# Kernel optimization log

Measured on AMD Instinct MI355X. Metric: run time of the kernel, lower is better.

The kernel has to match this reference:

```python
import jax, jax.numpy as jnp
import numpy as np

VOCAB = 2048
HID = 1024
BATCH = 64
STEPS = 512


def setup_inputs() -> dict:
    key = jax.random.key(0)
    ks = jax.random.split(key, 4)
    return {
        "X": jax.random.randint(ks[0], (BATCH, STEPS), 0, VOCAB, dtype=jnp.int64 if jax.config.read('jax_enable_x64') else jnp.int32),
        "state_h": jnp.zeros((BATCH, HID), dtype=jnp.float32),
        "W_xh": jax.random.normal(ks[1], (VOCAB, HID), dtype=jnp.float32) * 0.01,
        "W_hh": jax.random.normal(ks[2], (HID, HID), dtype=jnp.float32) * 0.01,
        "b_h": jnp.zeros((HID,), dtype=jnp.float32),
        "W_hq": jax.random.normal(ks[3], (HID, VOCAB), dtype=jnp.float32) * 0.01,
        "b_q": jnp.zeros((VOCAB,), dtype=jnp.float32),
    }


def reference(X, state_h, W_xh, W_hh, b_h, W_hq, b_q):
    # X: [B, T] int; one-hot of X.T -> [T, B, V] float32 (as in F.one_hot(X.T, V))
    Xoh = jax.nn.one_hot(X.T, VOCAB, dtype=jnp.float32)

    def step(H, x_t):
        # x_t: [B, V]; H: [B, H]
        H_new = jnp.tanh(x_t @ W_xh + H @ W_hh + b_h)
        Y_t = H_new @ W_hq + b_q  # [B, V]
        return H_new, Y_t

    H_final, Ys = jax.lax.scan(step, state_h, Xoh)  # Ys: [T, B, V]
    # torch.cat(outputs, dim=0) -> [T*B, V]
    Y = Ys.reshape(STEPS * BATCH, VOCAB)
    return Y, H_final
```

## Files before the change

kernel.cpp:

```cpp
#include <hip/hip_runtime.h>
#include <hip/hip_bf16.h>


#define BSZ  64
#define TSTEPS 512
#define HID  1024
#define VOC  2048

typedef __attribute__((ext_vector_type(8))) __bf16 bf16x8;
typedef __attribute__((ext_vector_type(4))) float  f32x4;

#define HALL_BYTES  67239936ull
#define WT_BYTES     4194304ull
#define FLAGS_BYTES   131328ull

__device__ inline void async_load16(const void* g, void* l) {
    __builtin_amdgcn_global_load_lds(
        (const __attribute__((address_space(1))) void*)g,
        (__attribute__((address_space(3))) void*)l, 16, 0, 0);
}

__device__ inline void load8_l2(const __hip_bfloat16* base, bf16x8* a) {
    asm volatile(
        "global_load_dwordx4 %0, %8, off sc0\n\t"
        "global_load_dwordx4 %1, %8, off offset:64 sc0\n\t"
        "global_load_dwordx4 %2, %8, off offset:128 sc0\n\t"
        "global_load_dwordx4 %3, %8, off offset:192 sc0\n\t"
        "global_load_dwordx4 %4, %8, off offset:256 sc0\n\t"
        "global_load_dwordx4 %5, %8, off offset:320 sc0\n\t"
        "global_load_dwordx4 %6, %8, off offset:384 sc0\n\t"
        "global_load_dwordx4 %7, %8, off offset:448 sc0"
        : "=&v"(a[0]), "=&v"(a[1]), "=&v"(a[2]), "=&v"(a[3]),
          "=&v"(a[4]), "=&v"(a[5]), "=&v"(a[6]), "=&v"(a[7])
        : "v"(base)
        : "memory");
}

__device__ inline void store_bf16_wt(__hip_bfloat16* p, float v) {
    const __hip_bfloat16 hv = __float2bfloat16(v);
    __hip_atomic_store((unsigned short*)p, __builtin_bit_cast(unsigned short, hv),
                       __ATOMIC_RELAXED, __HIP_MEMORY_SCOPE_SYSTEM);
}

__global__ __launch_bounds__(256, 1) void rnn_phase1(
    const int* __restrict__ X, const float* __restrict__ h0,
    const float* __restrict__ W_xh, const float* __restrict__ W_hh,
    const float* __restrict__ b_h,
    __hip_bfloat16* __restrict__ Hall, float* __restrict__ Hfin,
    unsigned int* __restrict__ flags)
{
    __builtin_amdgcn_fence(__ATOMIC_ACQUIRE, "agent");

    const int wg   = blockIdx.x;
    const int j0   = wg * 16;
    const int tid  = threadIdx.x;
    const int wave = tid >> 6;
    const int lane = tid & 63;
    const int lrow = lane & 15;
    const int lq   = lane >> 4;
    const int row0 = wave * 16;

    bf16x8 Bfr[32];
#pragma unroll
    for (int ks = 0; ks < 32; ++ks) {
        const int kb = ks * 32 + lq * 8;
        bf16x8 v;
#pragma unroll
        for (int j = 0; j < 8; ++j)
            v[j] = (__bf16)W_hh[(size_t)(kb + j) * HID + j0 + lrow];
        Bfr[ks] = v;
    }
    const float bh = b_h[j0 + lrow];

    for (int i = tid; i < BSZ * 16; i += 256) {
        const int b = i >> 4, c = i & 15;
        store_bf16_wt(Hall + (size_t)b * HID + j0 + c, h0[(size_t)b * HID + j0 + c]);
    }
    asm volatile("s_waitcnt vmcnt(0)" ::: "memory");
    __syncthreads();
    if (tid == 0)
        __hip_atomic_store(&flags[wg], 1u, __ATOMIC_RELAXED, __HIP_MEMORY_SCOPE_SYSTEM);

    for (int t = 0; t < TSTEPS; ++t) {
        float g[4];
#pragma unroll
        for (int r = 0; r < 4; ++r) {
            const int b = row0 + lq * 4 + r;
            const int x = X[b * TSTEPS + t];
            g[r] = W_xh[(size_t)x * HID + j0 + lrow];
        }
        {
            unsigned int* fl = flags + (size_t)t * 64;
            int guard = 0;
            while (__hip_atomic_load(&fl[lane], __ATOMIC_RELAXED, __HIP_MEMORY_SCOPE_SYSTEM) == 0u) {
                __builtin_amdgcn_s_sleep(1);
                if (++guard > (1 << 13)) break;
            }
        }

        const __hip_bfloat16* Arow =
            Hall + (size_t)t * (BSZ * HID) + (size_t)(row0 + lrow) * HID + lq * 8;
        bf16x8 a[32];
        load8_l2(Arow,       a);
        load8_l2(Arow + 256, a + 8);
        load8_l2(Arow + 512, a + 16);
        load8_l2(Arow + 768, a + 24);
        asm volatile("s_waitcnt vmcnt(0)" ::: "memory");
        __builtin_amdgcn_sched_barrier(0);

        f32x4 acc0 = {0.f, 0.f, 0.f, 0.f};
        f32x4 acc1 = {0.f, 0.f, 0.f, 0.f};
        f32x4 acc2 = {0.f, 0.f, 0.f, 0.f};
        f32x4 acc3 = {0.f, 0.f, 0.f, 0.f};
#pragma unroll
        for (int i = 0; i < 8; ++i) {
            acc0 = __builtin_amdgcn_mfma_f32_16x16x32_bf16(a[4 * i],     Bfr[4 * i],     acc0, 0, 0, 0);
            acc1 = __builtin_amdgcn_mfma_f32_16x16x32_bf16(a[4 * i + 1], Bfr[4 * i + 1], acc1, 0, 0, 0);
            acc2 = __builtin_amdgcn_mfma_f32_16x16x32_bf16(a[4 * i + 2], Bfr[4 * i + 2], acc2, 0, 0, 0);
            acc3 = __builtin_amdgcn_mfma_f32_16x16x32_bf16(a[4 * i + 3], Bfr[4 * i + 3], acc3, 0, 0, 0);
        }

        __hip_bfloat16* Hn = Hall + (size_t)(t + 1) * (BSZ * HID);
#pragma unroll
        for (int r = 0; r < 4; ++r) {
            const int b = row0 + lq * 4 + r;
            const float v = tanhf((acc0[r] + acc1[r]) + (acc2[r] + acc3[r]) + g[r] + bh);
            store_bf16_wt(Hn + (size_t)b * HID + j0 + lrow, v);
            if (t == TSTEPS - 1) Hfin[(size_t)b * HID + j0 + lrow] = v;
        }
        asm volatile("s_waitcnt vmcnt(0)" ::: "memory");
        __syncthreads();
        if (tid == 0)
            __hip_atomic_store(&flags[(size_t)(t + 1) * 64 + wg], 1u,
                               __ATOMIC_RELAXED, __HIP_MEMORY_SCOPE_SYSTEM);
    }
}

__global__ __launch_bounds__(256) void transpose_whq(
    const float* __restrict__ Whq, __hip_bfloat16* __restrict__ Wt)
{
    __shared__ float tile[32][33];
    const int n0 = blockIdx.x * 32, k0 = blockIdx.y * 32;
    const int tx = threadIdx.x & 31, ty = threadIdx.x >> 5;
    for (int yy = ty; yy < 32; yy += 8)
        tile[yy][tx] = Whq[(size_t)(k0 + yy) * VOC + n0 + tx];
    __syncthreads();
    for (int yy = ty; yy < 32; yy += 8)
        Wt[(size_t)(n0 + yy) * HID + k0 + tx] = __float2bfloat16(tile[tx][yy]);
}

__global__ __launch_bounds__(256, 2) void gemm_phase2(
    const __hip_bfloat16* __restrict__ A, const __hip_bfloat16* __restrict__ Bt,
    const float* __restrict__ b_q, float* __restrict__ Y)
{
    __shared__ __attribute__((aligned(16))) char As[16384];
    __shared__ __attribute__((aligned(16))) char Bs[16384];
    const int tid  = threadIdx.x;
    const int wave = tid >> 6, lane = tid & 63;
    const int m0 = blockIdx.y * 128, n0 = blockIdx.x * 128;
    const int wm = (wave >> 1) * 64, wn = (wave & 1) * 64;
    const int l15 = lane & 15, lq = lane >> 4;
    const int rsub = lane >> 3;
    const int bb   = (lane & 7) ^ (rsub & 7);

    f32x4 acc[4][4] = {};

    for (int kt = 0; kt < 16; ++kt) {
        __syncthreads();
#pragma unroll
        for (int i = 0; i < 4; ++i) {
            const int ii = wave * 4 + i;
            const size_t koff = (size_t)kt * 64 + bb * 8;
            async_load16(A  + (size_t)(m0 + ii * 8 + rsub) * HID + koff, As + ii * 1024);
            async_load16(Bt + (size_t)(n0 + ii * 8 + rsub) * HID + koff, Bs + ii * 1024);
        }
        __syncthreads();
#pragma unroll
        for (int ks = 0; ks < 2; ++ks) {
            bf16x8 af[4], bf[4];
#pragma unroll
            for (int mi = 0; mi < 4; ++mi) {
                const int row  = wm + mi * 16 + l15;
                const int slot = row * 8 + ((ks * 4 + lq) ^ (row & 7));
                af[mi] = *(const bf16x8*)(As + slot * 16);
            }
#pragma unroll
            for (int ni = 0; ni < 4; ++ni) {
                const int row  = wn + ni * 16 + l15;
                const int slot = row * 8 + ((ks * 4 + lq) ^ (row & 7));
                bf[ni] = *(const bf16x8*)(Bs + slot * 16);
            }
#pragma unroll
            for (int mi = 0; mi < 4; ++mi)
#pragma unroll
                for (int ni = 0; ni < 4; ++ni)
                    acc[mi][ni] = __builtin_amdgcn_mfma_f32_16x16x32_bf16(
                        af[mi], bf[ni], acc[mi][ni], 0, 0, 0);
        }
    }

    float bqv[4];
#pragma unroll
    for (int ni = 0; ni < 4; ++ni) bqv[ni] = b_q[n0 + wn + ni * 16 + l15];
#pragma unroll
    for (int mi = 0; mi < 4; ++mi)
#pragma unroll
        for (int r = 0; r < 4; ++r) {
            const int row = m0 + wm + mi * 16 + lq * 4 + r;
            float* yr = Y + (size_t)row * VOC + n0 + wn + l15;
#pragma unroll
            for (int ni = 0; ni < 4; ++ni)
                yr[ni * 16] = acc[mi][ni][r] + bqv[ni];
        }
}

extern "C" void kernel_launch(void* const* d_in, const int* in_sizes, int n_in,
                              void* d_out, int out_size, void* d_ws, size_t ws_size,
                              hipStream_t stream) {
    const int*   X    = (const int*)  d_in[0];
    const float* h0   = (const float*)d_in[1];
    const float* W_xh = (const float*)d_in[2];
    const float* W_hh = (const float*)d_in[3];
    const float* b_h  = (const float*)d_in[4];
    const float* W_hq = (const float*)d_in[5];
    const float* b_q  = (const float*)d_in[6];

    float* Y    = (float*)d_out;
    float* Hfin = Y + (size_t)TSTEPS * BSZ * VOC;

    char* ws = (char*)d_ws;
    __hip_bfloat16* Hall  = (__hip_bfloat16*)ws;
    __hip_bfloat16* Wt    = (__hip_bfloat16*)(ws + HALL_BYTES);
    unsigned int*   flags = (unsigned int*)(ws + HALL_BYTES + WT_BYTES);

    hipMemsetAsync(flags, 0, FLAGS_BYTES, stream);
    transpose_whq<<<dim3(VOC / 32, HID / 32), 256, 0, stream>>>(W_hq, Wt);
    rnn_phase1<<<64, 256, 0, stream>>>(X, h0, W_xh, W_hh, b_h, Hall, Hfin, flags);
    gemm_phase2<<<dim3(VOC / 128, (TSTEPS * BSZ) / 128), 256, 0, stream>>>(
        Hall + (size_t)BSZ * HID, Wt, b_q, Y);
}
```

Before: 3.373 ms.

## Pin recurrent workgroups to one XCC and use agent-scope stores

Launches 512 workgroups and keeps only the first 64 that land on XCC 0, assigning their logical slot through an atomic counter. With every participant on one die, the per-step hidden-state exchange and flag polling can stay in that die's shared L2 instead of crossing dies. The bf16 hidden stores are relaxed from system to agent scope to make them cheaper. The risks are relying on XCC 0 receiving at least 64 workgroups that are all co-resident (launch_bounds now allows 2 per CU), extra launch overhead from the discarded workgroups, and the dropped acquire fence.

```diff
diff --git a/kernel.cpp b/kernel.cpp
--- a/kernel.cpp
+++ b/kernel.cpp
@@ -36,22 +36,33 @@
         : "memory");
 }
 
-__device__ inline void store_bf16_wt(__hip_bfloat16* p, float v) {
+__device__ inline void store_bf16_l2(__hip_bfloat16* p, float v) {
     const __hip_bfloat16 hv = __float2bfloat16(v);
     __hip_atomic_store((unsigned short*)p, __builtin_bit_cast(unsigned short, hv),
-                       __ATOMIC_RELAXED, __HIP_MEMORY_SCOPE_SYSTEM);
-}
-
-__global__ __launch_bounds__(256, 1) void rnn_phase1(
+                       __ATOMIC_RELAXED, __HIP_MEMORY_SCOPE_AGENT);
+}
+
+__global__ __launch_bounds__(256, 2) void rnn_phase1(
     const int* __restrict__ X, const float* __restrict__ h0,
     const float* __restrict__ W_xh, const float* __restrict__ W_hh,
     const float* __restrict__ b_h,
     __hip_bfloat16* __restrict__ Hall, float* __restrict__ Hfin,
-    unsigned int* __restrict__ flags)
+    unsigned int* __restrict__ flags, unsigned int* __restrict__ slotctr)
 {
-    __builtin_amdgcn_fence(__ATOMIC_ACQUIRE, "agent");
-
-    const int wg   = blockIdx.x;
+    __shared__ int s_slot;
+    if (threadIdx.x == 0) {
+        unsigned int xcc;
+        asm volatile("s_getreg_b32 %0, hwreg(HW_REG_XCC_ID)" : "=s"(xcc));
+        int slot = -1;
+        if (xcc == 0)
+            slot = (int)__hip_atomic_fetch_add(slotctr, 1u, __ATOMIC_RELAXED,
+                                               __HIP_MEMORY_SCOPE_SYSTEM);
+        s_slot = slot;
+    }
+    __syncthreads();
+    const int wg = s_slot;
+    if (wg < 0 || wg >= 64) return;
+
     const int j0   = wg * 16;
     const int tid  = threadIdx.x;
     const int wave = tid >> 6;
@@ -74,7 +85,7 @@
 
     for (int i = tid; i < BSZ * 16; i += 256) {
         const int b = i >> 4, c = i & 15;
-        store_bf16_wt(Hall + (size_t)b * HID + j0 + c, h0[(size_t)b * HID + j0 + c]);
+        store_bf16_l2(Hall + (size_t)b * HID + j0 + c, h0[(size_t)b * HID + j0 + c]);
     }
     asm volatile("s_waitcnt vmcnt(0)" ::: "memory");
     __syncthreads();
@@ -125,7 +136,7 @@
         for (int r = 0; r < 4; ++r) {
             const int b = row0 + lq * 4 + r;
             const float v = tanhf((acc0[r] + acc1[r]) + (acc2[r] + acc3[r]) + g[r] + bh);
-            store_bf16_wt(Hn + (size_t)b * HID + j0 + lrow, v);
+            store_bf16_l2(Hn + (size_t)b * HID + j0 + lrow, v);
             if (t == TSTEPS - 1) Hfin[(size_t)b * HID + j0 + lrow] = v;
         }
         asm volatile("s_waitcnt vmcnt(0)" ::: "memory");
@@ -229,13 +240,14 @@
     float* Hfin = Y + (size_t)TSTEPS * BSZ * VOC;
 
     char* ws = (char*)d_ws;
-    __hip_bfloat16* Hall  = (__hip_bfloat16*)ws;
-    __hip_bfloat16* Wt    = (__hip_bfloat16*)(ws + HALL_BYTES);
-    unsigned int*   flags = (unsigned int*)(ws + HALL_BYTES + WT_BYTES);
-
-    hipMemsetAsync(flags, 0, FLAGS_BYTES, stream);
+    __hip_bfloat16* Hall    = (__hip_bfloat16*)ws;
+    __hip_bfloat16* Wt      = (__hip_bfloat16*)(ws + HALL_BYTES);
+    unsigned int*   flags   = (unsigned int*)(ws + HALL_BYTES + WT_BYTES);
+    unsigned int*   slotctr = (unsigned int*)(ws + HALL_BYTES + WT_BYTES + FLAGS_BYTES);
+
+    hipMemsetAsync(flags, 0, FLAGS_BYTES + 128, stream);
     transpose_whq<<<dim3(VOC / 32, HID / 32), 256, 0, stream>>>(W_hq, Wt);
-    rnn_phase1<<<64, 256, 0, stream>>>(X, h0, W_xh, W_hh, b_h, Hall, Hfin, flags);
+    rnn_phase1<<<512, 256, 0, stream>>>(X, h0, W_xh, W_hh, b_h, Hall, Hfin, flags, slotctr);
     gemm_phase2<<<dim3(VOC / 128, (TSTEPS * BSZ) / 128), 256, 0, stream>>>(
         Hall + (size_t)BSZ * HID, Wt, b_q, Y);
 }
```

Result: slower. 8.194 ms (+143.0%).
